# Kernel optimization log

Measured on AMD Instinct MI355X. Metric: run time of the kernel, lower is better.

Reference implementation:

```python
import jax, jax.numpy as jnp
import numpy as np
from jax import lax


def _interp_matrix(n_in: int, n_out: int) -> jnp.ndarray:
    """Row-stochastic [n_out, n_in] matrix for 1-D linear interp, align_corners=True."""
    if n_in == 1:
        return jnp.ones((n_out, 1), dtype=jnp.float32)
    pos = jnp.arange(n_out, dtype=jnp.float32) * ((n_in - 1) / (n_out - 1))
    lo = jnp.clip(jnp.floor(pos).astype(jnp.int32), 0, n_in - 2)
    frac = pos - lo.astype(jnp.float32)
    rows = jnp.arange(n_out)
    W = jnp.zeros((n_out, n_in), dtype=jnp.float32)
    W = W.at[rows, lo].add(1.0 - frac)
    W = W.at[rows, lo + 1].add(frac)
    return W


def setup_inputs() -> dict:
    key = jax.random.key(0)
    ks = jax.random.split(key, 10)
    B, C, H, W = 8, 64, 128, 128
    Ch = C // 2
    x = jax.random.normal(ks[0], (B, C, H, W), dtype=jnp.float32)
    # fan-in scaled weights to keep softmax logits in a sane range
    pool_w = jax.random.normal(ks[1], (C, C, 3, 3), dtype=jnp.float32) / np.sqrt(C * 9)
    pool_b = jax.random.normal(ks[2], (C,), dtype=jnp.float32) * 0.1
    q_w = jax.random.normal(ks[3], (Ch, C), dtype=jnp.float32) / np.sqrt(C)
    q_b = jax.random.normal(ks[4], (Ch,), dtype=jnp.float32) * 0.1
    k_w = jax.random.normal(ks[5], (Ch, C), dtype=jnp.float32) / np.sqrt(C)
    k_b = jax.random.normal(ks[6], (Ch,), dtype=jnp.float32) * 0.1
    v_w = jax.random.normal(ks[7], (C, C), dtype=jnp.float32) / np.sqrt(C)
    v_b = jax.random.normal(ks[8], (C,), dtype=jnp.float32) * 0.1
    gamma = jax.random.normal(ks[9], (1,), dtype=jnp.float32)
    return {"x": x, "pool_w": pool_w, "pool_b": pool_b, "q_w": q_w, "q_b": q_b,
            "k_w": k_w, "k_b": k_b, "v_w": v_w, "v_b": v_b, "gamma": gamma}


def reference(x, pool_w, pool_b, q_w, q_b, k_w, k_b, v_w, v_b, gamma):
    # 3x3 stride-2 pad-1 conv (the 'pool')
    xp = lax.conv_general_dilated(x, pool_w, window_strides=(2, 2),
                                  padding=((1, 1), (1, 1)),
                                  dimension_numbers=('NCHW', 'OIHW', 'NCHW'))
    xp = xp + pool_b[None, :, None, None]
    B, C, h, w = xp.shape
    N = h * w
    xf = xp.reshape(B, C, N)  # [B, C, N]
    # 1x1 convs as matmuls over the channel dim
    q = jnp.einsum('oc,bcn->bon', q_w, xf) + q_b[None, :, None]   # [B, C/2, N]
    k = jnp.einsum('oc,bcn->bon', k_w, xf) + k_b[None, :, None]   # [B, C/2, N]
    v = jnp.einsum('oc,bcn->bon', v_w, xf) + v_b[None, :, None]   # [B, C, N]
    # energy[b, n, m] = <q[:, n], k[:, m]>  -> softmax over m
    energy = jnp.einsum('bdn,bdm->bnm', q, k)                     # [B, N, N]
    attn = jax.nn.softmax(energy, axis=-1)
    # out = value @ attention^T  (torch: bmm(v, attn.permute(0,2,1)))
    out = jnp.einsum('bcm,bnm->bcn', v, attn).reshape(B, C, h, w)
    out = gamma[0] * out
    # bilinear upsample to input size, align_corners=True (separable matmuls)
    H, Wd = x.shape[2], x.shape[3]
    Wh = _interp_matrix(h, H)
    Ww = _interp_matrix(w, Wd)
    out = jnp.einsum('Hh,bchw->bcHw', Wh, out)
    out = jnp.einsum('Ww,bchw->bchW', Ww, out)
    return out + x
```

## Files before the change

kernel.cpp:

```cpp
#include <hip/hip_runtime.h>


typedef __attribute__((ext_vector_type(8))) short bf16x8;
typedef __attribute__((ext_vector_type(4))) float f32x4;

#define DEV static __device__ __forceinline__

DEV unsigned f2bf(float f) {
  union { float f; unsigned u; } a; a.f = f;
  return (a.u + 0x7FFFu + ((a.u >> 16) & 1u)) >> 16;
}
DEV float u2f(unsigned u) { union { unsigned u; float f; } a; a.u = u; return a.f; }
DEV unsigned cvtpk(float lo, float hi) {
  unsigned r;
  asm("v_cvt_pk_bf16_f32 %0, %1, %2" : "=v"(r) : "v"(lo), "v"(hi));
  return r;
}
DEV bf16x8 mk_bf16x8(unsigned w0, unsigned w1, unsigned w2, unsigned w3) {
  union { unsigned u[4]; bf16x8 v; } x;
  x.u[0] = w0; x.u[1] = w1; x.u[2] = w2; x.u[3] = w3;
  return x.v;
}
DEV void gload_lds16(const void* g, void* l) {
  __builtin_amdgcn_global_load_lds(
      (const __attribute__((address_space(1))) void*)g,
      (__attribute__((address_space(3))) void*)l, 16, 0, 0);
}

__global__ __launch_bounds__(256) void prep_kernel(
    const float* __restrict__ pw, const float* __restrict__ qw,
    const float* __restrict__ kw, const float* __restrict__ vw,
    const float* __restrict__ qb, const float* __restrict__ kb,
    const float* __restrict__ vb,
    unsigned short* __restrict__ Ag, unsigned short* __restrict__ A2g,
    float* __restrict__ bias2) {
  const float LOG2E = 1.4426950408889634f;
  const int i = blockIdx.x * 256 + threadIdx.x;
  if (i < 36864) {
    const int oc = i / 576, k = i - oc * 576;
    const int tap = k >> 6, ic = k & 63;
    Ag[i] = (unsigned short)f2bf(pw[(oc * 64 + ic) * 9 + tap]);
  }
  const int j = i - 36864;
  if (j >= 0 && j < 8192) {
    const int r = j >> 6, c = j & 63;
    if (r < 32)       A2g[j] = (unsigned short)f2bf(qw[r * 64 + c] * LOG2E);
    else if (r < 64)  A2g[j] = (unsigned short)f2bf(kw[(r - 32) * 64 + c]);
    else              A2g[j] = (unsigned short)f2bf(vw[(r - 64) * 64 + c]);
  }
  if (j >= 8192 && j < 8320) {
    const int r = j - 8192;
    bias2[r] = r < 32 ? qb[r] * LOG2E : (r < 64 ? kb[r - 32] : vb[r - 64]);
  }
}

__global__ __launch_bounds__(256) void convqkv_kernel(
    const float* __restrict__ x, const unsigned short* __restrict__ Ag,
    const float* __restrict__ pool_b, const unsigned short* __restrict__ A2g,
    const float* __restrict__ bias2,
    unsigned short* __restrict__ qT, unsigned short* __restrict__ kT,
    unsigned short* __restrict__ vM) {
  const int b = blockIdx.x >> 6, oy = blockIdx.x & 63;
  const int t = threadIdx.x, w = t >> 6, lane = t & 63;
  const int lr = lane & 15, lg = lane >> 4;
  __shared__ unsigned short sIn[390 * 64];
  __shared__ unsigned short sXP[64 * 64];
  char* sInB = (char*)sIn;
  char* sXPB = (char*)sXP;

  bf16x8 af[18];
  {
    const unsigned short* ap = Ag + (w * 16 + lr) * 576 + (lg << 3);
    #pragma unroll
    for (int kc = 0; kc < 18; ++kc)
      af[kc] = *(const bf16x8*)(ap + kc * 32);
  }

  #pragma unroll
  for (int rr = 0; rr < 2; ++rr) {
    const int pos = t + rr * 256;
    if (pos < 390) {
      const int ky = pos / 130, xi = pos - ky * 130;
      const int iy = 2 * oy + ky - 1, ix = xi - 1;
      const bool ok = (iy >= 0) & (iy < 128) & (ix >= 0) & (ix < 128);
      const float* xs = x + ((size_t)(b * 64) * 128 + (ok ? iy : 0)) * 128 +
                        (ok ? ix : 0);
      const int sw = pos & 7;
      #pragma unroll
      for (int o = 0; o < 8; ++o) {
        float f[8];
        #pragma unroll
        for (int jj = 0; jj < 8; ++jj)
          f[jj] = ok ? xs[(size_t)(o * 8 + jj) * 16384] : 0.f;
        bf16x8 v = mk_bf16x8(cvtpk(f[0], f[1]), cvtpk(f[2], f[3]),
                             cvtpk(f[4], f[5]), cvtpk(f[6], f[7]));
        *(bf16x8*)(sInB + pos * 128 + ((o ^ sw) << 4)) = v;
      }
    }
  }
  __syncthreads();

  f32x4 acc[4];
  #pragma unroll
  for (int nt = 0; nt < 4; ++nt) acc[nt] = (f32x4){0.f, 0.f, 0.f, 0.f};
  #pragma unroll
  for (int kc = 0; kc < 18; ++kc) {
    const int tap = kc >> 1, ky = tap / 3, kx = tap - ky * 3;
    const int o = ((kc & 1) << 2) + lg;
    #pragma unroll
    for (int nt = 0; nt < 4; ++nt) {
      const int xi = 2 * (nt * 16 + lr) + kx;
      const int pos = ky * 130 + xi;
      bf16x8 bfr = *(const bf16x8*)(sInB + pos * 128 + ((o ^ (pos & 7)) << 4));
      acc[nt] = __builtin_amdgcn_mfma_f32_16x16x32_bf16(af[kc], bfr, acc[nt],
                                                        0, 0, 0);
    }
  }

  const int ocBase = w * 16 + (lg << 2);
  float pb[4];
  #pragma unroll
  for (int r = 0; r < 4; ++r) pb[r] = pool_b[ocBase + r];
  const int ocOct = ocBase >> 3;
  const int withinB = (ocBase & 7) * 2;
  #pragma unroll
  for (int nt = 0; nt < 4; ++nt) {
    const int pos = nt * 16 + lr;
    const unsigned p01 = cvtpk(acc[nt][0] + pb[0], acc[nt][1] + pb[1]);
    const unsigned p23 = cvtpk(acc[nt][2] + pb[2], acc[nt][3] + pb[3]);
    char* base = sXPB + pos * 128 + ((ocOct ^ (pos & 7)) << 4) + withinB;
    *(unsigned*)(base) = p01;
    *(unsigned*)(base + 4) = p23;
  }
  __syncthreads();

  bf16x8 a2[2][2];
  #pragma unroll
  for (int mt = 0; mt < 2; ++mt)
    #pragma unroll
    for (int kc2 = 0; kc2 < 2; ++kc2)
      a2[mt][kc2] = *(const bf16x8*)(A2g + ((2 * w + mt) * 16 + lr) * 64 +
                                     kc2 * 32 + (lg << 3));
  f32x4 acc2[2][4];
  #pragma unroll
  for (int mt = 0; mt < 2; ++mt)
    #pragma unroll
    for (int nt = 0; nt < 4; ++nt) acc2[mt][nt] = (f32x4){0.f, 0.f, 0.f, 0.f};
  #pragma unroll
  for (int kc2 = 0; kc2 < 2; ++kc2) {
    const int o2 = (kc2 << 2) + lg;
    #pragma unroll
    for (int nt = 0; nt < 4; ++nt) {
      const int pos = nt * 16 + lr;
      bf16x8 bfr = *(const bf16x8*)(sXPB + pos * 128 + ((o2 ^ (pos & 7)) << 4));
      acc2[0][nt] = __builtin_amdgcn_mfma_f32_16x16x32_bf16(a2[0][kc2], bfr,
                                                            acc2[0][nt], 0, 0, 0);
      acc2[1][nt] = __builtin_amdgcn_mfma_f32_16x16x32_bf16(a2[1][kc2], bfr,
                                                            acc2[1][nt], 0, 0, 0);
    }
  }

  const int n0g = oy << 6;
  #pragma unroll
  for (int mt = 0; mt < 2; ++mt) {
    const int rowB = (2 * w + mt) * 16 + (lg << 2);
    float b2[4];
    #pragma unroll
    for (int r = 0; r < 4; ++r) b2[r] = bias2[rowB + r];
    if (rowB < 32) {
      #pragma unroll
      for (int nt = 0; nt < 4; ++nt) {
        const int n = n0g + nt * 16 + lr;
        unsigned* dst = (unsigned*)(qT + (((size_t)(b << 12) + n) << 5) + rowB);
        dst[0] = cvtpk(acc2[mt][nt][0] + b2[0], acc2[mt][nt][1] + b2[1]);
        dst[1] = cvtpk(acc2[mt][nt][2] + b2[2], acc2[mt][nt][3] + b2[3]);
      }
    } else if (rowB < 64) {
      #pragma unroll
      for (int nt = 0; nt < 4; ++nt) {
        const int n = n0g + nt * 16 + lr;
        unsigned* dst = (unsigned*)(kT + (((size_t)(b << 12) + n) << 5) + rowB - 32);
        dst[0] = cvtpk(acc2[mt][nt][0] + b2[0], acc2[mt][nt][1] + b2[1]);
        dst[1] = cvtpk(acc2[mt][nt][2] + b2[2], acc2[mt][nt][3] + b2[3]);
      }
    } else {
      const int cv = rowB - 64;
      #pragma unroll
      for (int nt = 0; nt < 4; ++nt) {
        const int n = n0g + nt * 16 + lr;
        #pragma unroll
        for (int r = 0; r < 4; ++r)
          vM[(((size_t)(b << 6) + cv + r) << 12) + n] =
              (unsigned short)f2bf(acc2[mt][nt][r] + b2[r]);
      }
    }
  }
}

template <int NSPLIT>
__global__ __launch_bounds__(256, 2) void attn_kernel(
    const unsigned short* __restrict__ qT, const unsigned short* __restrict__ kT,
    const unsigned short* __restrict__ vM,
    unsigned short* __restrict__ Pb, float* __restrict__ Lbuf) {
  constexpr int CH = 64 / NSPLIT;
  __shared__ char lds[24576];
  __shared__ char Plds[4][9216];
  const int t = threadIdx.x, w = t >> 6, lane = t & 63;
  const int lr = lane & 15, lg = lane >> 4;
  const int b = blockIdx.x & 7;
  const int u = (blockIdx.x >> 3) & 15;
  const int s = blockIdx.x >> 7;
  const int n0 = (u << 8) + (w << 6);
  const int kb0 = s * (CH << 6);
  char* Pw = Plds[w];

  bf16x8 bq[4];
  #pragma unroll
  for (int nt = 0; nt < 4; ++nt)
    bq[nt] = *(const bf16x8*)(
        qT + (((size_t)(b << 12) + n0 + nt * 16 + lr) << 5) + (lg << 3));

  const unsigned short* ksrc = kT + ((size_t)b << 17);
  const unsigned short* vsrcb = vM + ((size_t)b << 18);

  f32x4 acc[4][4];
  #pragma unroll
  for (int nt = 0; nt < 4; ++nt)
    #pragma unroll
    for (int ct = 0; ct < 4; ++ct) acc[nt][ct] = (f32x4){0.f, 0.f, 0.f, 0.f};
  float l_run[4] = {0.f, 0.f, 0.f, 0.f};

  const int vsw = (lane & 7) ^ ((lane >> 3) & 7);
  const int klocal = (w << 4) + (lane >> 2);
  const int kseg = (lane & 3) ^ ((klocal >> 1) & 3);

  #define STAGE(ci_) {                                                         \
    const int kb_ = kb0 + (((ci_) & (CH - 1)) << 6);                           \
    char* sb_ = lds + ((ci_) & 1) * 12288;                                     \
    gload_lds16((const void*)(ksrc + (((size_t)(kb_ + klocal)) << 5) +         \
                  (kseg << 3)),                                                \
                sb_ + (w << 10));                                              \
    gload_lds16((const void*)(vsrcb +                                          \
                  (((size_t)((w << 4) + (lane >> 3))) << 12) + kb_ +           \
                  (vsw << 3)),                                                 \
                sb_ + 4096 + (w << 11));                                       \
    gload_lds16((const void*)(vsrcb +                                          \
                  (((size_t)((w << 4) + 8 + (lane >> 3))) << 12) + kb_ +       \
                  (vsw << 3)),                                                 \
                sb_ + 4096 + (w << 11) + 1024);                                \
  }

  STAGE(0);

  for (int cc = 0; cc < CH; ++cc) {
    asm volatile("s_waitcnt vmcnt(0)" ::: "memory");
    __builtin_amdgcn_s_barrier();
    __builtin_amdgcn_sched_barrier(0);
    if (cc + 1 < CH) STAGE(cc + 1);
    char* base = lds + (cc & 1) * 12288;

    f32x4 st[4][4];
    const f32x4 z4 = {0.f, 0.f, 0.f, 0.f};
    __builtin_amdgcn_s_setprio(1);
    #pragma unroll
    for (int j = 0; j < 4; ++j) {
      const int key = 16 * j + lr;
      const bf16x8 ka = *(const bf16x8*)(
          base + (key << 6) + ((lg ^ ((key >> 1) & 3)) << 4));
      #pragma unroll
      for (int nt = 0; nt < 4; ++nt)
        st[nt][j] = __builtin_amdgcn_mfma_f32_16x16x32_bf16(ka, bq[nt], z4,
                                                            0, 0, 0);
    }
    __builtin_amdgcn_s_setprio(0);

    #pragma unroll
    for (int nt = 0; nt < 4; ++nt) {
      float ps0 = 0.f, ps1 = 0.f;
      #pragma unroll
      for (int j = 0; j < 4; ++j) {
        const float p0 = __builtin_amdgcn_exp2f(st[nt][j][0]);
        const float p1 = __builtin_amdgcn_exp2f(st[nt][j][1]);
        const float p2 = __builtin_amdgcn_exp2f(st[nt][j][2]);
        const float p3 = __builtin_amdgcn_exp2f(st[nt][j][3]);
        ps0 += p0 + p1;
        ps1 += p2 + p3;
        *(uint2*)(Pw + (nt * 16 + lr) * 144 + (((j << 2) + lg) << 3)) =
            (uint2){cvtpk(p0, p1), cvtpk(p2, p3)};
      }
      l_run[nt] += ps0 + ps1;
    }

    #pragma unroll
    for (int h = 0; h < 2; ++h) {
      bf16x8 vr[4];
      #pragma unroll
      for (int ct = 0; ct < 4; ++ct) {
        const int c = (ct << 4) + lr;
        const int o = (h << 2) + lg;
        vr[ct] = *(const bf16x8*)(base + 4096 + (c << 7) +
                                  ((o ^ (lr & 7)) << 4));
      }
      #pragma unroll
      for (int nt = 0; nt < 4; ++nt) {
        const bf16x8 pbf = *(const bf16x8*)(
            Pw + (nt * 16 + lr) * 144 + (((h << 3) + (lg << 1)) << 3));
        __builtin_amdgcn_s_setprio(1);
        #pragma unroll
        for (int ct = 0; ct < 4; ++ct)
          acc[nt][ct] = __builtin_amdgcn_mfma_f32_16x16x32_bf16(vr[ct], pbf,
                                                                acc[nt][ct],
                                                                0, 0, 0);
        __builtin_amdgcn_s_setprio(0);
      }
    }
  }

  #pragma unroll
  for (int nt = 0; nt < 4; ++nt) {
    l_run[nt] += __shfl_xor(l_run[nt], 16, 64);
    l_run[nt] += __shfl_xor(l_run[nt], 32, 64);
  }

  unsigned short* dst = Pb + ((size_t)s << 21);
  #pragma unroll
  for (int nt = 0; nt < 4; ++nt) {
    const int q = n0 + nt * 16 + lr;
    #pragma unroll
    for (int ct = 0; ct < 4; ++ct)
      #pragma unroll
      for (int r = 0; r < 4; ++r) {
        const int c = (ct << 4) + (lg << 2) + r;
        dst[((size_t)((b << 6) + c) << 12) + q] =
            (unsigned short)f2bf(acc[nt][ct][r]);
      }
  }
  if (lane < 16) {
    #pragma unroll
    for (int nt = 0; nt < 4; ++nt)
      Lbuf[((size_t)(s * 8 + b) << 12) + n0 + nt * 16 + lane] = l_run[nt];
  }
  #undef STAGE
}

template <int NSPLIT>
__global__ __launch_bounds__(256) void merge_kernel(
    const unsigned short* __restrict__ Pb, const float* __restrict__ Lbuf,
    const float* __restrict__ gamma_p, float* __restrict__ attnP) {
  const int idx = blockIdx.x * 256 + threadIdx.x;
  const int n0 = (idx & 511) << 3;
  const int c = (idx >> 9) & 63;
  const int b = idx >> 15;
  const size_t base = ((size_t)((b << 6) + c) << 12) + n0;

  float num[8] = {0.f, 0.f, 0.f, 0.f, 0.f, 0.f, 0.f, 0.f};
  #pragma unroll
  for (int s = 0; s < NSPLIT; ++s) {
    const uint4 v = *(const uint4*)(Pb + ((size_t)s << 21) + base);
    num[0] += u2f(v.x << 16); num[1] += u2f(v.x & 0xffff0000u);
    num[2] += u2f(v.y << 16); num[3] += u2f(v.y & 0xffff0000u);
    num[4] += u2f(v.z << 16); num[5] += u2f(v.z & 0xffff0000u);
    num[6] += u2f(v.w << 16); num[7] += u2f(v.w & 0xffff0000u);
  }
  float den[8] = {0.f, 0.f, 0.f, 0.f, 0.f, 0.f, 0.f, 0.f};
  #pragma unroll
  for (int s = 0; s < NSPLIT; ++s) {
    const float* lp = Lbuf + (((size_t)(s * 8 + b)) << 12) + n0;
    const f32x4 l0 = *(const f32x4*)lp;
    const f32x4 l1 = *(const f32x4*)(lp + 4);
    #pragma unroll
    for (int j = 0; j < 4; ++j) { den[j] += l0[j]; den[4 + j] += l1[j]; }
  }
  const float g = gamma_p[0];
  f32x4 o0, o1;
  #pragma unroll
  for (int j = 0; j < 4; ++j) {
    o0[j] = g * num[j] / den[j];
    o1[j] = g * num[4 + j] / den[4 + j];
  }
  *(f32x4*)(attnP + base) = o0;
  *(f32x4*)(attnP + base + 4) = o1;
}

__global__ __launch_bounds__(256) void upsample_residual_kernel(
    const float* __restrict__ attn_out, const float* __restrict__ x,
    float* __restrict__ out) {
  const int idx = blockIdx.x * 256 + threadIdx.x;
  const int X0 = (idx & 31) << 2;
  int rem = idx >> 5;
  const int Y = rem & 127; rem >>= 7;
  const int c = rem & 63;
  const int b = rem >> 6;

  const float sr = 63.0f / 127.0f;
  float fy = Y * sr;
  int iy = (int)fy; if (iy > 62) iy = 62;
  const float ty = fy - (float)iy;
  const float* ap = attn_out + (((size_t)(b * 64 + c)) << 12);
  const float* r0 = ap + iy * 64;
  const float* r1 = r0 + 64;

  float tmp[4];
  #pragma unroll
  for (int k = 0; k < 4; ++k) {
    const int X = X0 + k;
    float fx = X * sr;
    int ix = (int)fx; if (ix > 62) ix = 62;
    const float tx = fx - (float)ix;
    float v0 = r0[ix] + tx * (r0[ix + 1] - r0[ix]);
    float v1 = r1[ix] + tx * (r1[ix + 1] - r1[ix]);
    tmp[k] = v0 + ty * (v1 - v0);
  }
  const size_t o = (((size_t)((b * 64 + c) * 128 + Y)) << 7) + X0;
  f32x4 xv = *reinterpret_cast<const f32x4*>(x + o);
  f32x4 ov = {tmp[0] + xv[0], tmp[1] + xv[1], tmp[2] + xv[2], tmp[3] + xv[3]};
  *reinterpret_cast<f32x4*>(out + o) = ov;
}

extern "C" void kernel_launch(void* const* d_in, const int* in_sizes, int n_in,
                              void* d_out, int out_size, void* d_ws, size_t ws_size,
                              hipStream_t stream) {
  const float* x      = (const float*)d_in[0];
  const float* pool_w = (const float*)d_in[1];
  const float* pool_b = (const float*)d_in[2];
  const float* q_w    = (const float*)d_in[3];
  const float* q_b    = (const float*)d_in[4];
  const float* k_w    = (const float*)d_in[5];
  const float* k_b    = (const float*)d_in[6];
  const float* v_w    = (const float*)d_in[7];
  const float* v_b    = (const float*)d_in[8];
  const float* gamma  = (const float*)d_in[9];
  float* out = (float*)d_out;

  char* ws = (char*)d_ws;
  unsigned short* Ag   = (unsigned short*)(ws);
  unsigned short* A2g  = (unsigned short*)(ws + 81920);
  float* bias2         = (float*)(ws + 98304);
  unsigned short* qT   = (unsigned short*)(ws + 1048576);
  unsigned short* kT   = (unsigned short*)(ws + 3145728);
  unsigned short* vM   = (unsigned short*)(ws + 5242880);
  unsigned short* Pb   = (unsigned short*)(ws + 9437184);
  float* attnP         = (float*)(ws + 1048576);

  prep_kernel<<<177, 256, 0, stream>>>(pool_w, q_w, k_w, v_w, q_b, k_b, v_b,
                                       Ag, A2g, bias2);
  convqkv_kernel<<<512, 256, 0, stream>>>(x, Ag, pool_b, A2g, bias2, qT, kT, vM);

  if (ws_size >= 44040192u) {
    float* Lbuf = (float*)(ws + 9437184 + 8 * 4194304);
    attn_kernel<8><<<1024, 256, 0, stream>>>(qT, kT, vM, Pb, Lbuf);
    merge_kernel<8><<<1024, 256, 0, stream>>>(Pb, Lbuf, gamma, attnP);
  } else {
    float* Lbuf = (float*)(ws + 9437184 + 4 * 4194304);
    attn_kernel<4><<<512, 256, 0, stream>>>(qT, kT, vM, Pb, Lbuf);
    merge_kernel<4><<<1024, 256, 0, stream>>>(Pb, Lbuf, gamma, attnP);
  }
  upsample_residual_kernel<<<8192, 256, 0, stream>>>(attnP, x, out);
}
```

Before: 90.90 us.

## Fuse split-merge with upsample-residual and halve attention P staging LDS

The merge of split-K attention partials and the bilinear upsample plus residual are combined into one kernel. Each block normalises one (batch, channel) 64x64 map into shared memory and then writes the 128x128 upsampled output directly, which removes the fp32 attnP round trip through global memory and one launch. Separately, the attention inner loop now processes query tiles in two halves, so the per-wave P staging buffer in LDS shrinks to half. This may allow more blocks per CU but adds a serial dependency between the halves. The fused kernel runs only 512 blocks, each doing 16 strided iterations, so it has less parallelism than the old 8192-block upsample.

```diff
diff --git a/kernel.cpp b/kernel.cpp
--- a/kernel.cpp
+++ b/kernel.cpp
@@ -204,7 +204,7 @@
     unsigned short* __restrict__ Pb, float* __restrict__ Lbuf) {
   constexpr int CH = 64 / NSPLIT;
   __shared__ char lds[24576];
-  __shared__ char Plds[4][9216];
+  __shared__ char Plds[4][4608];
   const int t = threadIdx.x, w = t >> 6, lane = t & 63;
   const int lr = lane & 15, lg = lane >> 4;
   const int b = blockIdx.x & 7;
@@ -259,59 +259,61 @@
     if (cc + 1 < CH) STAGE(cc + 1);
     char* base = lds + (cc & 1) * 12288;
 
-    f32x4 st[4][4];
-    const f32x4 z4 = {0.f, 0.f, 0.f, 0.f};
-    __builtin_amdgcn_s_setprio(1);
-    #pragma unroll
-    for (int j = 0; j < 4; ++j) {
-      const int key = 16 * j + lr;
-      const bf16x8 ka = *(const bf16x8*)(
-          base + (key << 6) + ((lg ^ ((key >> 1) & 3)) << 4));
-      #pragma unroll
-      for (int nt = 0; nt < 4; ++nt)
-        st[nt][j] = __builtin_amdgcn_mfma_f32_16x16x32_bf16(ka, bq[nt], z4,
-                                                            0, 0, 0);
-    }
-    __builtin_amdgcn_s_setprio(0);
-
-    #pragma unroll
-    for (int nt = 0; nt < 4; ++nt) {
-      float ps0 = 0.f, ps1 = 0.f;
+    #pragma unroll
+    for (int p = 0; p < 2; ++p) {
+      f32x4 st[2][4];
+      const f32x4 z4 = {0.f, 0.f, 0.f, 0.f};
+      __builtin_amdgcn_s_setprio(1);
       #pragma unroll
       for (int j = 0; j < 4; ++j) {
-        const float p0 = __builtin_amdgcn_exp2f(st[nt][j][0]);
-        const float p1 = __builtin_amdgcn_exp2f(st[nt][j][1]);
-        const float p2 = __builtin_amdgcn_exp2f(st[nt][j][2]);
-        const float p3 = __builtin_amdgcn_exp2f(st[nt][j][3]);
-        ps0 += p0 + p1;
-        ps1 += p2 + p3;
-        *(uint2*)(Pw + (nt * 16 + lr) * 144 + (((j << 2) + lg) << 3)) =
-            (uint2){cvtpk(p0, p1), cvtpk(p2, p3)};
-      }
-      l_run[nt] += ps0 + ps1;
-    }
-
-    #pragma unroll
-    for (int h = 0; h < 2; ++h) {
-      bf16x8 vr[4];
-      #pragma unroll
-      for (int ct = 0; ct < 4; ++ct) {
-        const int c = (ct << 4) + lr;
-        const int o = (h << 2) + lg;
-        vr[ct] = *(const bf16x8*)(base + 4096 + (c << 7) +
-                                  ((o ^ (lr & 7)) << 4));
-      }
-      #pragma unroll
-      for (int nt = 0; nt < 4; ++nt) {
-        const bf16x8 pbf = *(const bf16x8*)(
-            Pw + (nt * 16 + lr) * 144 + (((h << 3) + (lg << 1)) << 3));
-        __builtin_amdgcn_s_setprio(1);
+        const int key = 16 * j + lr;
+        const bf16x8 ka = *(const bf16x8*)(
+            base + (key << 6) + ((lg ^ ((key >> 1) & 3)) << 4));
+        st[0][j] = __builtin_amdgcn_mfma_f32_16x16x32_bf16(ka, bq[2 * p], z4,
+                                                           0, 0, 0);
+        st[1][j] = __builtin_amdgcn_mfma_f32_16x16x32_bf16(ka, bq[2 * p + 1],
+                                                           z4, 0, 0, 0);
+      }
+      __builtin_amdgcn_s_setprio(0);
+
+      #pragma unroll
+      for (int q = 0; q < 2; ++q) {
+        float ps0 = 0.f, ps1 = 0.f;
         #pragma unroll
-        for (int ct = 0; ct < 4; ++ct)
-          acc[nt][ct] = __builtin_amdgcn_mfma_f32_16x16x32_bf16(vr[ct], pbf,
-                                                                acc[nt][ct],
-                                                                0, 0, 0);
-        __builtin_amdgcn_s_setprio(0);
+        for (int j = 0; j < 4; ++j) {
+          const float p0 = __builtin_amdgcn_exp2f(st[q][j][0]);
+          const float p1 = __builtin_amdgcn_exp2f(st[q][j][1]);
+          const float p2 = __builtin_amdgcn_exp2f(st[q][j][2]);
+          const float p3 = __builtin_amdgcn_exp2f(st[q][j][3]);
+          ps0 += p0 + p1;
+          ps1 += p2 + p3;
+          *(uint2*)(Pw + (q * 16 + lr) * 144 + (((j << 2) + lg) << 3)) =
+              (uint2){cvtpk(p0, p1), cvtpk(p2, p3)};
+        }
+        l_run[2 * p + q] += ps0 + ps1;
+      }
+
+      #pragma unroll
+      for (int h = 0; h < 2; ++h) {
+        bf16x8 vr[4];
+        #pragma unroll
+        for (int ct = 0; ct < 4; ++ct) {
+          const int c = (ct << 4) + lr;
+          const int o = (h << 2) + lg;
+          vr[ct] = *(const bf16x8*)(base + 4096 + (c << 7) +
+                                    ((o ^ (lr & 7)) << 4));
+        }
+        #pragma unroll
+        for (int q = 0; q < 2; ++q) {
+          const bf16x8 pbf = *(const bf16x8*)(
+              Pw + (q * 16 + lr) * 144 + (((h << 3) + (lg << 1)) << 3));
+          __builtin_amdgcn_s_setprio(1);
+          #pragma unroll
+          for (int ct = 0; ct < 4; ++ct)
+            acc[2 * p + q][ct] = __builtin_amdgcn_mfma_f32_16x16x32_bf16(
+                vr[ct], pbf, acc[2 * p + q][ct], 0, 0, 0);
+          __builtin_amdgcn_s_setprio(0);
+        }
       }
     }
   }
@@ -344,77 +346,69 @@
 }
 
 template <int NSPLIT>
-__global__ __launch_bounds__(256) void merge_kernel(
+__global__ __launch_bounds__(256) void merge_upsample_kernel(
     const unsigned short* __restrict__ Pb, const float* __restrict__ Lbuf,
-    const float* __restrict__ gamma_p, float* __restrict__ attnP) {
-  const int idx = blockIdx.x * 256 + threadIdx.x;
-  const int n0 = (idx & 511) << 3;
-  const int c = (idx >> 9) & 63;
-  const int b = idx >> 15;
-  const size_t base = ((size_t)((b << 6) + c) << 12) + n0;
-
-  float num[8] = {0.f, 0.f, 0.f, 0.f, 0.f, 0.f, 0.f, 0.f};
-  #pragma unroll
-  for (int s = 0; s < NSPLIT; ++s) {
-    const uint4 v = *(const uint4*)(Pb + ((size_t)s << 21) + base);
-    num[0] += u2f(v.x << 16); num[1] += u2f(v.x & 0xffff0000u);
-    num[2] += u2f(v.y << 16); num[3] += u2f(v.y & 0xffff0000u);
-    num[4] += u2f(v.z << 16); num[5] += u2f(v.z & 0xffff0000u);
-    num[6] += u2f(v.w << 16); num[7] += u2f(v.w & 0xffff0000u);
-  }
-  float den[8] = {0.f, 0.f, 0.f, 0.f, 0.f, 0.f, 0.f, 0.f};
-  #pragma unroll
-  for (int s = 0; s < NSPLIT; ++s) {
-    const float* lp = Lbuf + (((size_t)(s * 8 + b)) << 12) + n0;
-    const f32x4 l0 = *(const f32x4*)lp;
-    const f32x4 l1 = *(const f32x4*)(lp + 4);
-    #pragma unroll
-    for (int j = 0; j < 4; ++j) { den[j] += l0[j]; den[4 + j] += l1[j]; }
-  }
+    const float* __restrict__ gamma_p, const float* __restrict__ x,
+    float* __restrict__ out) {
+  __shared__ float sA[4096];
+  const int t = threadIdx.x;
+  const int b = blockIdx.x >> 6, c = blockIdx.x & 63;
   const float g = gamma_p[0];
-  f32x4 o0, o1;
-  #pragma unroll
-  for (int j = 0; j < 4; ++j) {
-    o0[j] = g * num[j] / den[j];
-    o1[j] = g * num[4 + j] / den[4 + j];
-  }
-  *(f32x4*)(attnP + base) = o0;
-  *(f32x4*)(attnP + base + 4) = o1;
-}
-
-__global__ __launch_bounds__(256) void upsample_residual_kernel(
-    const float* __restrict__ attn_out, const float* __restrict__ x,
-    float* __restrict__ out) {
-  const int idx = blockIdx.x * 256 + threadIdx.x;
-  const int X0 = (idx & 31) << 2;
-  int rem = idx >> 5;
-  const int Y = rem & 127; rem >>= 7;
-  const int c = rem & 63;
-  const int b = rem >> 6;
+  const size_t basebc = ((size_t)((b << 6) + c) << 12);
+
+  #pragma unroll
+  for (int i = 0; i < 2; ++i) {
+    const int n0 = (t + (i << 8)) << 3;
+    float num[8] = {0.f, 0.f, 0.f, 0.f, 0.f, 0.f, 0.f, 0.f};
+    #pragma unroll
+    for (int s = 0; s < NSPLIT; ++s) {
+      const uint4 v = *(const uint4*)(Pb + ((size_t)s << 21) + basebc + n0);
+      num[0] += u2f(v.x << 16); num[1] += u2f(v.x & 0xffff0000u);
+      num[2] += u2f(v.y << 16); num[3] += u2f(v.y & 0xffff0000u);
+      num[4] += u2f(v.z << 16); num[5] += u2f(v.z & 0xffff0000u);
+      num[6] += u2f(v.w << 16); num[7] += u2f(v.w & 0xffff0000u);
+    }
+    float den[8] = {0.f, 0.f, 0.f, 0.f, 0.f, 0.f, 0.f, 0.f};
+    #pragma unroll
+    for (int s = 0; s < NSPLIT; ++s) {
+      const float* lp = Lbuf + (((size_t)(s * 8 + b)) << 12) + n0;
+      const f32x4 l0 = *(const f32x4*)lp;
+      const f32x4 l1 = *(const f32x4*)(lp + 4);
+      #pragma unroll
+      for (int j = 0; j < 4; ++j) { den[j] += l0[j]; den[4 + j] += l1[j]; }
+    }
+    #pragma unroll
+    for (int j = 0; j < 8; ++j) sA[n0 + j] = g * num[j] / den[j];
+  }
+  __syncthreads();
 
   const float sr = 63.0f / 127.0f;
-  float fy = Y * sr;
-  int iy = (int)fy; if (iy > 62) iy = 62;
-  const float ty = fy - (float)iy;
-  const float* ap = attn_out + (((size_t)(b * 64 + c)) << 12);
-  const float* r0 = ap + iy * 64;
-  const float* r1 = r0 + 64;
-
-  float tmp[4];
-  #pragma unroll
-  for (int k = 0; k < 4; ++k) {
-    const int X = X0 + k;
-    float fx = X * sr;
-    int ix = (int)fx; if (ix > 62) ix = 62;
-    const float tx = fx - (float)ix;
-    float v0 = r0[ix] + tx * (r0[ix + 1] - r0[ix]);
-    float v1 = r1[ix] + tx * (r1[ix + 1] - r1[ix]);
-    tmp[k] = v0 + ty * (v1 - v0);
-  }
-  const size_t o = (((size_t)((b * 64 + c) * 128 + Y)) << 7) + X0;
-  f32x4 xv = *reinterpret_cast<const f32x4*>(x + o);
-  f32x4 ov = {tmp[0] + xv[0], tmp[1] + xv[1], tmp[2] + xv[2], tmp[3] + xv[3]};
-  *reinterpret_cast<f32x4*>(out + o) = ov;
+  const float* xb = x + (((size_t)((b << 6) + c)) << 14);
+  float* ob = out + (((size_t)((b << 6) + c)) << 14);
+  for (int k = 0; k < 16; ++k) {
+    const int qid = t + (k << 8);
+    const int Y = qid >> 5, X0 = (qid & 31) << 2;
+    const float fy = Y * sr;
+    int iy = (int)fy; if (iy > 62) iy = 62;
+    const float ty = fy - (float)iy;
+    const float* r0 = sA + iy * 64;
+    const float* r1 = r0 + 64;
+    float tmp[4];
+    #pragma unroll
+    for (int kk = 0; kk < 4; ++kk) {
+      const int X = X0 + kk;
+      const float fx = X * sr;
+      int ix = (int)fx; if (ix > 62) ix = 62;
+      const float tx = fx - (float)ix;
+      const float v0 = r0[ix] + tx * (r0[ix + 1] - r0[ix]);
+      const float v1 = r1[ix] + tx * (r1[ix + 1] - r1[ix]);
+      tmp[kk] = v0 + ty * (v1 - v0);
+    }
+    const size_t o = ((size_t)Y << 7) + X0;
+    const f32x4 xv = *(const f32x4*)(xb + o);
+    f32x4 ov = {tmp[0] + xv[0], tmp[1] + xv[1], tmp[2] + xv[2], tmp[3] + xv[3]};
+    *(f32x4*)(ob + o) = ov;
+  }
 }
 
 extern "C" void kernel_launch(void* const* d_in, const int* in_sizes, int n_in,
@@ -440,7 +434,6 @@
   unsigned short* kT   = (unsigned short*)(ws + 3145728);
   unsigned short* vM   = (unsigned short*)(ws + 5242880);
   unsigned short* Pb   = (unsigned short*)(ws + 9437184);
-  float* attnP         = (float*)(ws + 1048576);
 
   prep_kernel<<<177, 256, 0, stream>>>(pool_w, q_w, k_w, v_w, q_b, k_b, v_b,
                                        Ag, A2g, bias2);
@@ -449,11 +442,10 @@
   if (ws_size >= 44040192u) {
     float* Lbuf = (float*)(ws + 9437184 + 8 * 4194304);
     attn_kernel<8><<<1024, 256, 0, stream>>>(qT, kT, vM, Pb, Lbuf);
-    merge_kernel<8><<<1024, 256, 0, stream>>>(Pb, Lbuf, gamma, attnP);
+    merge_upsample_kernel<8><<<512, 256, 0, stream>>>(Pb, Lbuf, gamma, x, out);
   } else {
     float* Lbuf = (float*)(ws + 9437184 + 4 * 4194304);
     attn_kernel<4><<<512, 256, 0, stream>>>(qT, kT, vM, Pb, Lbuf);
-    merge_kernel<4><<<1024, 256, 0, stream>>>(Pb, Lbuf, gamma, attnP);
-  }
-  upsample_residual_kernel<<<8192, 256, 0, stream>>>(attnP, x, out);
-}
+    merge_upsample_kernel<4><<<512, 256, 0, stream>>>(Pb, Lbuf, gamma, x, out);
+  }
+}
```

Measured after the change: 83.10 us (median of 2 runs). 1.09x faster.
